# Kernel tuning notes

Hardware: AMD Instinct MI355X
Metric: run time of the kernel (lower is better)

Reference implementation:

```python
import jax, jax.numpy as jnp
import numpy as np

EPS = 1e-5

def _conv(x, w, b, stride, pad):
    y = jax.lax.conv_general_dilated(
        x, w, window_strides=(stride, stride),
        padding=[(pad, pad), (pad, pad)],
        dimension_numbers=('NCHW', 'OIHW', 'NCHW'))
    return y + b.reshape(1, -1, 1, 1)

def _bn(x, gamma, beta):
    # training-mode batch norm: per-channel batch statistics over (N, H, W)
    mean = jnp.mean(x, axis=(0, 2, 3), keepdims=True)
    var = jnp.var(x, axis=(0, 2, 3), keepdims=True)
    xn = (x - mean) * jax.lax.rsqrt(var + EPS)
    return gamma.reshape(1, -1, 1, 1) * xn + beta.reshape(1, -1, 1, 1)

def setup_inputs() -> dict:
    key = jax.random.key(0)
    ks = jax.random.split(key, 8)
    N, Cin, H, W = 64, 1024, 14, 14
    P = 256                      # planes (bottleneck width)
    Cout = P * 4                 # expansion = 4 -> 1024
    def kaiming(k, shape):
        fan_in = shape[1] * shape[2] * shape[3]
        return jax.random.normal(k, shape, jnp.float32) * np.float32(np.sqrt(2.0 / fan_in))
    return {
        'x':  jax.random.normal(ks[0], (N, Cin, H, W), jnp.float32),
        'w1': kaiming(ks[1], (P, Cin, 1, 1)),  'b1': jnp.zeros((P,), jnp.float32),
        'g1': jnp.ones((P,), jnp.float32),     'be1': jnp.zeros((P,), jnp.float32),
        'w2': kaiming(ks[2], (P, P, 3, 3)),    'b2': jnp.zeros((P,), jnp.float32),
        'g2': jnp.ones((P,), jnp.float32),     'be2': jnp.zeros((P,), jnp.float32),
        'w3': kaiming(ks[3], (Cout, P, 1, 1)), 'b3': jnp.zeros((Cout,), jnp.float32),
        'g3': jnp.ones((Cout,), jnp.float32),  'be3': jnp.zeros((Cout,), jnp.float32),
        'residual_scale': jnp.zeros((1,), jnp.float32),
    }

def reference(x, w1, b1, g1, be1, w2, b2, g2, be2, w3, b3, g3, be3, residual_scale):
    out = jax.nn.relu(_bn(_conv(x, w1, b1, 1, 0), g1, be1))   # 1x1 reduce
    out = jax.nn.relu(_bn(_conv(out, w2, b2, 1, 1), g2, be2)) # 3x3
    out = _bn(_conv(out, w3, b3, 1, 0), g3, be3)              # 1x1 expand
    out = jax.nn.softplus(residual_scale)[0] * out            # scaled residual branch
    out = x + out                                             # identity shortcut (stride=1, Cin==Cout)
    return jax.nn.relu(out)
```

## Files before the change

kernel.cpp:

```cpp
#include <hip/hip_runtime.h>
#include <hip/hip_bf16.h>
#include <cstdint>

#define NB   64
#define CIN  1024
#define HWSP 196
#define MTOT 12544
#define PL   256
#define COUT 1024

using f32x4 = __attribute__((ext_vector_type(4))) float;
using s16x8 = __attribute__((ext_vector_type(8))) short;

static __device__ __forceinline__ short f2bf(float f) {
  union { __hip_bfloat16 h; short s; } u;
  u.h = __float2bfloat16(f);
  return u.s;
}
static __device__ __forceinline__ float bf2f(short s) {
  union { float f; unsigned u; } x;
  x.u = ((unsigned)(unsigned short)s) << 16;
  return x.f;
}

static __device__ __forceinline__ void gload16(const void* g, void* l) {
  __builtin_amdgcn_global_load_lds((const __attribute__((address_space(1))) void*)g,
                                   (__attribute__((address_space(3))) void*)l, 16, 0, 0);
}

__global__ __launch_bounds__(256) void k_prep(const float* __restrict__ x,
                                              const float* __restrict__ w1,
                                              const float* __restrict__ w2,
                                              const float* __restrict__ w3,
                                              short* __restrict__ xb,
                                              short* __restrict__ w1b,
                                              short* __restrict__ w2b,
                                              short* __restrict__ w3b,
                                              float* __restrict__ statszero) {
  const int bid = blockIdx.x;
  if (bid < 2048) {
    __shared__ float tile[32][197];
    const int n = bid >> 5;
    const int c0 = (bid & 31) * 32;
    for (int idx = threadIdx.x; idx < 32 * 196; idx += 256) {
      int cl = idx / 196, hw = idx % 196;
      tile[cl][hw] = x[((size_t)(n * CIN + c0 + cl)) * HWSP + hw];
    }
    __syncthreads();
    for (int idx = threadIdx.x; idx < 196 * 32; idx += 256) {
      int hw = idx >> 5, cl = idx & 31;
      xb[((size_t)(n * HWSP + hw)) * CIN + c0 + cl] = f2bf(tile[cl][hw]);
    }
  } else if (bid < 6400) {
    int i = (bid - 2048) * 256 + threadIdx.x;
    if (i < 262144) w1b[i] = f2bf(w1[i]);
    int j = i - 262144;
    if (j >= 0 && j < 589824) {
      int co = j / 2304, rem = j % 2304;
      int d = rem >> 8, ci = rem & 255;
      w2b[j] = f2bf(w2[((size_t)(co * 256 + ci)) * 9 + d]);
    }
    int k = i - 851968;
    if (k >= 0 && k < 262144) w3b[k] = f2bf(w3[k]);
  } else {
    for (int k = threadIdx.x; k < 3136; k += 256) statszero[k] = 0.f;
  }
}

static __device__ __forceinline__ int swz(int row, int k16) {
  return row * 128 + (((unsigned)(k16 ^ (row & 7))) << 4);
}

template <int MODE, int K>
__global__ __launch_bounds__(256) void gemm_kernel(const short* __restrict__ A,
                                                   const short* __restrict__ Bw,
                                                   const float* __restrict__ bias,
                                                   short* __restrict__ Yb,
                                                   float* __restrict__ st,
                                                   int Nc,
                                                   const short* __restrict__ zerobuf) {
  __shared__ __align__(16) char lds[2][32768];

  const int m0 = blockIdx.x * 128;
  const int n0 = blockIdx.y * 128;
  const int t = threadIdx.x;
  const int lane = t & 63, wid = t >> 6;
  const int wm = wid >> 1, wn = wid & 1;
  const int g = lane >> 4, r = lane & 15;
  constexpr int NKT = K >> 6;

  const short* aSrc[4];
  int aN[4], aH[4], aW[4], aCi[4];
  const short* bSrc[4];
#pragma unroll
  for (int q = 0; q < 4; ++q) {
    int chunk = t + q * 256;
    int row = chunk >> 3;
    int k16s = (chunk & 7) ^ (row & 7);
    if (MODE == 0) {
      aSrc[q] = A + (size_t)(m0 + row) * K + k16s * 8;
    } else {
      int m = m0 + row;
      int n_ = m / 196;
      int hw = m - n_ * 196;
      aN[q] = n_;
      aH[q] = hw / 14;
      aW[q] = hw - aH[q] * 14;
      aCi[q] = k16s * 8;
    }
    bSrc[q] = Bw + (size_t)(n0 + row) * K + k16s * 8;
  }

  auto stage = [&](int buf, int kt) {
    const int k0 = kt << 6;
    char* dA = &lds[buf][0];
    char* dB = &lds[buf][16384];
#pragma unroll
    for (int q = 0; q < 4; ++q) {
      const short* s;
      if (MODE == 0) {
        s = aSrc[q] + k0;
      } else {
        int d = kt >> 2;
        int dh = d / 3, dw = d - dh * 3;
        int hh = aH[q] + dh - 1, ww = aW[q] + dw - 1;
        s = ((unsigned)hh < 14u && (unsigned)ww < 14u)
                ? A + ((size_t)(aN[q] * 196 + hh * 14 + ww)) * 256 + (k0 & 255) + aCi[q]
                : zerobuf;
      }
      gload16(s, dA + (t + q * 256) * 16);
    }
#pragma unroll
    for (int q = 0; q < 4; ++q)
      gload16(bSrc[q] + k0, dB + (t + q * 256) * 16);
  };

  f32x4 acc[4][4] = {};
  auto compute = [&](int buf) {
    char* baseA = &lds[buf][0];
    char* baseB = &lds[buf][16384];
#pragma unroll
    for (int ks = 0; ks < 2; ++ks) {
      s16x8 af[4], bfr[4];
#pragma unroll
      for (int i = 0; i < 4; ++i)
        af[i] = *(const s16x8*)(baseA + swz(wm * 64 + i * 16 + r, ks * 4 + g));
#pragma unroll
      for (int j = 0; j < 4; ++j)
        bfr[j] = *(const s16x8*)(baseB + swz(wn * 64 + j * 16 + r, ks * 4 + g));
#pragma unroll
      for (int i = 0; i < 4; ++i)
#pragma unroll
        for (int j = 0; j < 4; ++j)
          acc[i][j] = __builtin_amdgcn_mfma_f32_16x16x32_bf16(af[i], bfr[j], acc[i][j], 0, 0, 0);
    }
  };

  stage(0, 0);
  int cur = 0;
#pragma unroll 1
  for (int kt = 0; kt < NKT - 1; ++kt) {
    stage(cur ^ 1, kt + 1);
    asm volatile("s_waitcnt vmcnt(8)" ::: "memory");
    __builtin_amdgcn_s_barrier();
    compute(cur);
    asm volatile("" ::: "memory");
    __builtin_amdgcn_s_barrier();
    cur ^= 1;
  }
  asm volatile("s_waitcnt vmcnt(0)" ::: "memory");
  __builtin_amdgcn_s_barrier();
  compute(cur);

#pragma unroll
  for (int j = 0; j < 4; ++j) {
    int col = n0 + wn * 64 + j * 16 + r;
    float bv = bias[col];
    float ps = 0.f, pq = 0.f;
#pragma unroll
    for (int i = 0; i < 4; ++i) {
      int row_base = m0 + wm * 64 + i * 16 + g * 4;
#pragma unroll
      for (int rr = 0; rr < 4; ++rr) {
        float v = acc[i][j][rr] + bv;
        ps += v;
        pq += v * v;
        Yb[(size_t)(row_base + rr) * Nc + col] = f2bf(v);
      }
    }
    ps += __shfl_xor(ps, 16);
    ps += __shfl_xor(ps, 32);
    pq += __shfl_xor(pq, 16);
    pq += __shfl_xor(pq, 32);
    if (lane < 16) {
      atomicAdd(&st[col], ps);
      atomicAdd(&st[Nc + col], pq);
    }
  }
}

__global__ __launch_bounds__(256) void k_apply(short* __restrict__ Yb,
                                               const float* __restrict__ st,
                                               const float* __restrict__ gamma,
                                               const float* __restrict__ beta) {
  __shared__ float lsc[256], lsh[256];
  const int t = threadIdx.x;
  {
    const float inv = 1.0f / 12544.0f;
    float mean = st[t] * inv;
    float var = st[256 + t] * inv - mean * mean;
    float s = gamma[t] * rsqrtf(var + 1e-5f);
    lsc[t] = s;
    lsh[t] = beta[t] - mean * s;
  }
  __syncthreads();
  size_t i8 = ((size_t)blockIdx.x * 256 + t) * 8;
  s16x8 v = *(const s16x8*)(Yb + i8);
  int c0 = (int)(i8 & 255);
#pragma unroll
  for (int e = 0; e < 8; ++e) {
    float f = bf2f(v[e]);
    v[e] = f2bf(fmaxf(lsc[c0 + e] * f + lsh[c0 + e], 0.f));
  }
  *(s16x8*)(Yb + i8) = v;
}

__global__ __launch_bounds__(256) void k_final(const float* __restrict__ x,
                                               const short* __restrict__ y3b,
                                               const float* __restrict__ st,
                                               const float* __restrict__ gamma,
                                               const float* __restrict__ beta,
                                               const float* __restrict__ rs,
                                               float* __restrict__ out) {
  __shared__ short ytile[64][198];
  __shared__ float lsc[64], lsh[64];
  const int n = blockIdx.x;
  const int co0 = blockIdx.y * 64;
  const int t = threadIdx.x;
  if (t < 64) {
    const float inv = 1.0f / 12544.0f;
    int c = co0 + t;
    float mean = st[c] * inv;
    float var = st[1024 + c] * inv - mean * mean;
    float s = gamma[c] * rsqrtf(var + 1e-5f);
    lsc[t] = s;
    lsh[t] = beta[c] - mean * s;
  }
#pragma unroll
  for (int iter = 0; iter < 49; ++iter) {
    int idx = iter * 256 + t;
    int hw = idx >> 6, c = idx & 63;
    ytile[c][hw] = y3b[((size_t)(n * 196 + hw)) * 1024 + co0 + c];
  }
  __syncthreads();
  float z = rs[0];
  float s = fmaxf(z, 0.f) + log1pf(expf(-fabsf(z)));
#pragma unroll
  for (int iter = 0; iter < 49; ++iter) {
    int idx = iter * 256 + t;
    int co = idx / 196, hw = idx - co * 196;
    size_t xi = ((size_t)(n * 1024 + co0 + co)) * 196 + hw;
    float v = bf2f(ytile[co][hw]);
    float o = x[xi] + s * (lsc[co] * v + lsh[co]);
    out[xi] = fmaxf(o, 0.f);
  }
}

extern "C" void kernel_launch(void* const* d_in, const int* in_sizes, int n_in,
                              void* d_out, int out_size, void* d_ws, size_t ws_size,
                              hipStream_t stream) {
  const float* x   = (const float*)d_in[0];
  const float* w1  = (const float*)d_in[1];
  const float* b1  = (const float*)d_in[2];
  const float* g1  = (const float*)d_in[3];
  const float* be1 = (const float*)d_in[4];
  const float* w2  = (const float*)d_in[5];
  const float* b2  = (const float*)d_in[6];
  const float* g2  = (const float*)d_in[7];
  const float* be2 = (const float*)d_in[8];
  const float* w3  = (const float*)d_in[9];
  const float* b3  = (const float*)d_in[10];
  const float* g3  = (const float*)d_in[11];
  const float* be3 = (const float*)d_in[12];
  const float* rs  = (const float*)d_in[13];
  float* out = (float*)d_out;
  char* ws = (char*)d_ws;

  size_t off = 0;
  auto alloc = [&](size_t bytes) {
    size_t o = off;
    off += (bytes + 255) & ~(size_t)255;
    return o;
  };
  short* xb  = (short*)(ws + alloc((size_t)MTOT * CIN * 2));
  short* w1b = (short*)(ws + alloc((size_t)262144 * 2));
  short* w2b = (short*)(ws + alloc((size_t)589824 * 2));
  short* w3b = (short*)(ws + alloc((size_t)262144 * 2));
  short* y1b = (short*)(ws + alloc((size_t)MTOT * PL * 2));
  short* y2b = (short*)(ws + alloc((size_t)MTOT * PL * 2));
  short* y3b = (short*)(ws + alloc((size_t)MTOT * COUT * 2));
  float* stats = (float*)(ws + alloc(12288 + 256));
  float* stat1 = stats, *stat2 = stats + 512, *stat3 = stats + 1024;
  short* zerobuf = (short*)(stats + 3072);

  k_prep<<<6401, 256, 0, stream>>>(x, w1, w2, w3, xb, w1b, w2b, w3b, stats);

  gemm_kernel<0, 1024><<<dim3(98, 2), 256, 0, stream>>>(xb, w1b, b1, y1b, stat1, 256, zerobuf);
  k_apply<<<1568, 256, 0, stream>>>(y1b, stat1, g1, be1);

  gemm_kernel<1, 2304><<<dim3(98, 2), 256, 0, stream>>>(y1b, w2b, b2, y2b, stat2, 256, zerobuf);
  k_apply<<<1568, 256, 0, stream>>>(y2b, stat2, g2, be2);

  gemm_kernel<0, 256><<<dim3(98, 8), 256, 0, stream>>>(y2b, w3b, b3, y3b, stat3, 1024, zerobuf);

  k_final<<<dim3(64, 16), 256, 0, stream>>>(x, y3b, stat3, g3, be3, rs, out);
}
```

Baseline: 122.6 us.

## Pre-pack weights into MFMA fragment order and load B directly into registers

The weight conversion kernel now writes w1/w2/w3 in a packed layout that matches the per-lane MFMA B-fragment order, grouped by 64-column tiles and K-steps. The GEMM kernel drops LDS staging for B: each wave loads its B fragments straight from global memory into registers with a register double buffer, and LDS is halved to hold only A. This removes LDS write/read traffic and bank pressure for B. In exchange it raises register pressure and makes the two waves sharing a column tile fetch the same B data redundantly from global memory or cache.

Result: no change. 123.4 us (+0.6%).

```diff
diff --git a/kernel.cpp b/kernel.cpp
--- a/kernel.cpp
+++ b/kernel.cpp
@@ -53,15 +53,30 @@
     }
   } else if (bid < 6400) {
     int i = (bid - 2048) * 256 + threadIdx.x;
-    if (i < 262144) w1b[i] = f2bf(w1[i]);
-    int j = i - 262144;
-    if (j >= 0 && j < 589824) {
-      int co = j / 2304, rem = j % 2304;
-      int d = rem >> 8, ci = rem & 255;
-      w2b[j] = f2bf(w2[((size_t)(co * 256 + ci)) * 9 + d]);
-    }
-    int k = i - 851968;
-    if (k >= 0 && k < 262144) w3b[k] = f2bf(w3[k]);
+    if (i < 262144) {
+      int e = i & 7, l = (i >> 3) & 63, j = (i >> 9) & 3, ks = (i >> 11) & 1;
+      int kt = (i >> 12) & 15, g64 = i >> 16;
+      int co = g64 * 64 + j * 16 + (l & 15);
+      int k = kt * 64 + ks * 32 + (l >> 4) * 8 + e;
+      w1b[i] = f2bf(w1[co * 1024 + k]);
+    }
+    int j2 = i - 262144;
+    if (j2 >= 0 && j2 < 589824) {
+      int e = j2 & 7, l = (j2 >> 3) & 63, j = (j2 >> 9) & 3, ks = (j2 >> 11) & 1;
+      int kt = (j2 >> 12) % 36, g64 = (j2 >> 12) / 36;
+      int co = g64 * 64 + j * 16 + (l & 15);
+      int k = kt * 64 + ks * 32 + (l >> 4) * 8 + e;
+      int d = k >> 8, ci = k & 255;
+      w2b[j2] = f2bf(w2[((size_t)(co * 256 + ci)) * 9 + d]);
+    }
+    int k3 = i - 851968;
+    if (k3 >= 0 && k3 < 262144) {
+      int e = k3 & 7, l = (k3 >> 3) & 63, j = (k3 >> 9) & 3, ks = (k3 >> 11) & 1;
+      int kt = (k3 >> 12) & 3, g64 = k3 >> 14;
+      int co = g64 * 64 + j * 16 + (l & 15);
+      int k = kt * 64 + ks * 32 + (l >> 4) * 8 + e;
+      w3b[k3] = f2bf(w3[co * 256 + k]);
+    }
   } else {
     for (int k = threadIdx.x; k < 3136; k += 256) statszero[k] = 0.f;
   }
@@ -73,25 +88,25 @@
 
 template <int MODE, int K>
 __global__ __launch_bounds__(256) void gemm_kernel(const short* __restrict__ A,
-                                                   const short* __restrict__ Bw,
+                                                   const short* __restrict__ Bp,
                                                    const float* __restrict__ bias,
                                                    short* __restrict__ Yb,
                                                    float* __restrict__ st,
                                                    int Nc,
                                                    const short* __restrict__ zerobuf) {
-  __shared__ __align__(16) char lds[2][32768];
+  __shared__ __align__(16) char lds[2][16384];
+  constexpr int NKT = K >> 6;
 
   const int m0 = blockIdx.x * 128;
-  const int n0 = blockIdx.y * 128;
   const int t = threadIdx.x;
   const int lane = t & 63, wid = t >> 6;
   const int wm = wid >> 1, wn = wid & 1;
   const int g = lane >> 4, r = lane & 15;
-  constexpr int NKT = K >> 6;
+  const int g64 = blockIdx.y * 2 + wn;
+  const short* bptr = Bp + (size_t)g64 * NKT * 4096 + lane * 8;
 
   const short* aSrc[4];
   int aN[4], aH[4], aW[4], aCi[4];
-  const short* bSrc[4];
 #pragma unroll
   for (int q = 0; q < 4; ++q) {
     int chunk = t + q * 256;
@@ -108,13 +123,11 @@
       aW[q] = hw - aH[q] * 14;
       aCi[q] = k16s * 8;
     }
-    bSrc[q] = Bw + (size_t)(n0 + row) * K + k16s * 8;
-  }
-
-  auto stage = [&](int buf, int kt) {
+  }
+
+  auto stageA = [&](int buf, int kt) {
     const int k0 = kt << 6;
     char* dA = &lds[buf][0];
-    char* dB = &lds[buf][16384];
 #pragma unroll
     for (int q = 0; q < 4; ++q) {
       const short* s;
@@ -130,51 +143,67 @@
       }
       gload16(s, dA + (t + q * 256) * 16);
     }
-#pragma unroll
-    for (int q = 0; q < 4; ++q)
-      gload16(bSrc[q] + k0, dB + (t + q * 256) * 16);
   };
 
+  auto loadB = [&](s16x8 (&br)[8], int kt) {
+    const short* p = bptr + (size_t)kt * 4096;
+#pragma unroll
+    for (int f = 0; f < 8; ++f)
+      br[f] = *(const s16x8*)(p + f * 512);
+  };
+
   f32x4 acc[4][4] = {};
-  auto compute = [&](int buf) {
+  auto compute = [&](int buf, const s16x8 (&br)[8]) {
     char* baseA = &lds[buf][0];
-    char* baseB = &lds[buf][16384];
 #pragma unroll
     for (int ks = 0; ks < 2; ++ks) {
-      s16x8 af[4], bfr[4];
+      s16x8 af[4];
 #pragma unroll
       for (int i = 0; i < 4; ++i)
         af[i] = *(const s16x8*)(baseA + swz(wm * 64 + i * 16 + r, ks * 4 + g));
 #pragma unroll
-      for (int j = 0; j < 4; ++j)
-        bfr[j] = *(const s16x8*)(baseB + swz(wn * 64 + j * 16 + r, ks * 4 + g));
-#pragma unroll
       for (int i = 0; i < 4; ++i)
 #pragma unroll
         for (int j = 0; j < 4; ++j)
-          acc[i][j] = __builtin_amdgcn_mfma_f32_16x16x32_bf16(af[i], bfr[j], acc[i][j], 0, 0, 0);
+          acc[i][j] = __builtin_amdgcn_mfma_f32_16x16x32_bf16(af[i], br[ks * 4 + j], acc[i][j], 0, 0, 0);
     }
   };
 
-  stage(0, 0);
-  int cur = 0;
+  s16x8 brA[8], brB[8];
+  loadB(brA, 0);
+  stageA(0, 0);
+  int kt = 0;
 #pragma unroll 1
-  for (int kt = 0; kt < NKT - 1; ++kt) {
-    stage(cur ^ 1, kt + 1);
-    asm volatile("s_waitcnt vmcnt(8)" ::: "memory");
+  for (kt = 0; kt + 2 < NKT; kt += 2) {
+    loadB(brB, kt + 1);
+    stageA(1, kt + 1);
+    asm volatile("s_waitcnt vmcnt(12)" ::: "memory");
     __builtin_amdgcn_s_barrier();
-    compute(cur);
+    compute(0, brA);
     asm volatile("" ::: "memory");
     __builtin_amdgcn_s_barrier();
-    cur ^= 1;
-  }
+    loadB(brA, kt + 2);
+    stageA(0, kt + 2);
+    asm volatile("s_waitcnt vmcnt(12)" ::: "memory");
+    __builtin_amdgcn_s_barrier();
+    compute(1, brB);
+    asm volatile("" ::: "memory");
+    __builtin_amdgcn_s_barrier();
+  }
+  loadB(brB, kt + 1);
+  stageA(1, kt + 1);
+  asm volatile("s_waitcnt vmcnt(12)" ::: "memory");
+  __builtin_amdgcn_s_barrier();
+  compute(0, brA);
+  asm volatile("" ::: "memory");
+  __builtin_amdgcn_s_barrier();
   asm volatile("s_waitcnt vmcnt(0)" ::: "memory");
   __builtin_amdgcn_s_barrier();
-  compute(cur);
+  compute(1, brB);
 
 #pragma unroll
   for (int j = 0; j < 4; ++j) {
-    int col = n0 + wn * 64 + j * 16 + r;
+    int col = blockIdx.y * 128 + wn * 64 + j * 16 + r;
     float bv = bias[col];
     float ps = 0.f, pq = 0.f;
 #pragma unroll
```

## Split-K the first two GEMMs and add a partial-sum reduction kernel

Applied to the files above, without the earlier changes.

The 1x1-reduce and 3x3 GEMMs launched only 196 blocks, which underfills the GPU's compute units. They now split the K dimension across 2 and 3 z-slices, write fp32 partial tiles to a workspace, and a new reduce kernel sums the partials, adds bias, writes the bf16 output and accumulates the BN statistics. The aim is more parallelism for these small-N GEMMs. In exchange it adds extra fp32 global traffic for the partials and one more kernel launch per stage.

New measurement: 135.6 us. 1.11x slower.

```diff
diff --git a/kernel.cpp b/kernel.cpp
--- a/kernel.cpp
+++ b/kernel.cpp
@@ -71,23 +71,26 @@
   return row * 128 + (((unsigned)(k16 ^ (row & 7))) << 4);
 }
 
-template <int MODE, int K>
+template <int MODE, int K, int SK>
 __global__ __launch_bounds__(256) void gemm_kernel(const short* __restrict__ A,
                                                    const short* __restrict__ Bw,
                                                    const float* __restrict__ bias,
                                                    short* __restrict__ Yb,
+                                                   float* __restrict__ Pp,
                                                    float* __restrict__ st,
                                                    int Nc,
                                                    const short* __restrict__ zerobuf) {
   __shared__ __align__(16) char lds[2][32768];
+  constexpr int NKT = K / 64 / SK;
 
   const int m0 = blockIdx.x * 128;
   const int n0 = blockIdx.y * 128;
+  const int sk = (SK > 1) ? blockIdx.z : 0;
+  const int kt0 = sk * NKT;
   const int t = threadIdx.x;
   const int lane = t & 63, wid = t >> 6;
   const int wm = wid >> 1, wn = wid & 1;
   const int g = lane >> 4, r = lane & 15;
-  constexpr int NKT = K >> 6;
 
   const short* aSrc[4];
   int aN[4], aH[4], aW[4], aCi[4];
@@ -156,11 +159,11 @@
     }
   };
 
-  stage(0, 0);
+  stage(0, kt0);
   int cur = 0;
 #pragma unroll 1
-  for (int kt = 0; kt < NKT - 1; ++kt) {
-    stage(cur ^ 1, kt + 1);
+  for (int kti = 0; kti < NKT - 1; ++kti) {
+    stage(cur ^ 1, kt0 + kti + 1);
     asm volatile("s_waitcnt vmcnt(8)" ::: "memory");
     __builtin_amdgcn_s_barrier();
     compute(cur);
@@ -172,31 +175,68 @@
   __builtin_amdgcn_s_barrier();
   compute(cur);
 
-#pragma unroll
-  for (int j = 0; j < 4; ++j) {
-    int col = n0 + wn * 64 + j * 16 + r;
-    float bv = bias[col];
-    float ps = 0.f, pq = 0.f;
-#pragma unroll
-    for (int i = 0; i < 4; ++i) {
-      int row_base = m0 + wm * 64 + i * 16 + g * 4;
-#pragma unroll
-      for (int rr = 0; rr < 4; ++rr) {
-        float v = acc[i][j][rr] + bv;
-        ps += v;
-        pq += v * v;
-        Yb[(size_t)(row_base + rr) * Nc + col] = f2bf(v);
+  if (SK == 1) {
+#pragma unroll
+    for (int j = 0; j < 4; ++j) {
+      int col = n0 + wn * 64 + j * 16 + r;
+      float bv = bias[col];
+      float ps = 0.f, pq = 0.f;
+#pragma unroll
+      for (int i = 0; i < 4; ++i) {
+        int row_base = m0 + wm * 64 + i * 16 + g * 4;
+#pragma unroll
+        for (int rr = 0; rr < 4; ++rr) {
+          float v = acc[i][j][rr] + bv;
+          ps += v;
+          pq += v * v;
+          Yb[(size_t)(row_base + rr) * Nc + col] = f2bf(v);
+        }
       }
-    }
-    ps += __shfl_xor(ps, 16);
-    ps += __shfl_xor(ps, 32);
-    pq += __shfl_xor(pq, 16);
-    pq += __shfl_xor(pq, 32);
-    if (lane < 16) {
-      atomicAdd(&st[col], ps);
-      atomicAdd(&st[Nc + col], pq);
-    }
-  }
+      ps += __shfl_xor(ps, 16);
+      ps += __shfl_xor(ps, 32);
+      pq += __shfl_xor(pq, 16);
+      pq += __shfl_xor(pq, 32);
+      if (lane < 16) {
+        atomicAdd(&st[col], ps);
+        atomicAdd(&st[Nc + col], pq);
+      }
+    }
+  } else {
+#pragma unroll
+    for (int j = 0; j < 4; ++j) {
+      int col = n0 + wn * 64 + j * 16 + r;
+#pragma unroll
+      for (int i = 0; i < 4; ++i) {
+        int row_base = m0 + wm * 64 + i * 16 + g * 4;
+#pragma unroll
+        for (int rr = 0; rr < 4; ++rr)
+          Pp[((size_t)sk * MTOT + row_base + rr) * Nc + col] = acc[i][j][rr];
+      }
+    }
+  }
+}
+
+template <int SKn>
+__global__ __launch_bounds__(256) void k_reduce(const float* __restrict__ Pp,
+                                                const float* __restrict__ bias,
+                                                short* __restrict__ Yb,
+                                                float* __restrict__ st) {
+  const int t = threadIdx.x;
+  const int r0 = blockIdx.x * 64;
+  const float bv = bias[t];
+  float s = 0.f, q = 0.f;
+  for (int rr = 0; rr < 64; ++rr) {
+    size_t row = r0 + rr;
+    float v = bv;
+#pragma unroll
+    for (int sk = 0; sk < SKn; ++sk)
+      v += Pp[((size_t)sk * MTOT + row) * 256 + t];
+    s += v;
+    q += v * v;
+    Yb[row * 256 + t] = f2bf(v);
+  }
+  atomicAdd(&st[t], s);
+  atomicAdd(&st[256 + t], q);
 }
 
 __global__ __launch_bounds__(256) void k_apply(short* __restrict__ Yb,
@@ -299,19 +339,25 @@
   short* y1b = (short*)(ws + alloc((size_t)MTOT * PL * 2));
   short* y2b = (short*)(ws + alloc((size_t)MTOT * PL * 2));
   short* y3b = (short*)(ws + alloc((size_t)MTOT * COUT * 2));
+  float* Pp  = (float*)(ws + alloc((size_t)3 * MTOT * 256 * 4));
   float* stats = (float*)(ws + alloc(12288 + 256));
   float* stat1 = stats, *stat2 = stats + 512, *stat3 = stats + 1024;
   short* zerobuf = (short*)(stats + 3072);
 
   k_prep<<<6401, 256, 0, stream>>>(x, w1, w2, w3, xb, w1b, w2b, w3b, stats);
 
-  gemm_kernel<0, 1024><<<dim3(98, 2), 256, 0, stream>>>(xb, w1b, b1, y1b, stat1, 256, zerobuf);
+  gemm_kernel<0, 1024, 2><<<dim3(98, 2, 2), 256, 0, stream>>>(
+      xb, w1b, b1, y1b, Pp, stat1, 256, zerobuf);
+  k_reduce<2><<<196, 256, 0, stream>>>(Pp, b1, y1b, stat1);
   k_apply<<<1568, 256, 0, stream>>>(y1b, stat1, g1, be1);
 
-  gemm_kernel<1, 2304><<<dim3(98, 2), 256, 0, stream>>>(y1b, w2b, b2, y2b, stat2, 256, zerobuf);
+  gemm_kernel<1, 2304, 3><<<dim3(98, 2, 3), 256, 0, stream>>>(
+      y1b, w2b, b2, y2b, Pp, stat2, 256, zerobuf);
+  k_reduce<3><<<196, 256, 0, stream>>>(Pp, b2, y2b, stat2);
   k_apply<<<1568, 256, 0, stream>>>(y2b, stat2, g2, be2);
 
-  gemm_kernel<0, 256><<<dim3(98, 8), 256, 0, stream>>>(y2b, w3b, b3, y3b, stat3, 1024, zerobuf);
+  gemm_kernel<0, 256, 1><<<dim3(98, 8, 1), 256, 0, stream>>>(
+      y2b, w3b, b3, y3b, Pp, stat3, 1024, zerobuf);
 
   k_final<<<dim3(64, 16), 256, 0, stream>>>(x, y3b, stat3, g3, be3, rs, out);
 }
```
